# Kernel optimization log

Hardware: AMD Instinct MI355X
Metric: run time of the kernel (lower is better)

## Reference

```python
import jax, jax.numpy as jnp
import numpy as np

T, B, I, N, C = 2048, 512, 28, 256, 2
TAU = 2.0

def _lin_init(key, out_f, in_f):
    # torch nn.Linear default: U(-1/sqrt(in_f), 1/sqrt(in_f)) for weight and bias
    s = 1.0 / np.sqrt(in_f)
    kw, kb = jax.random.split(key)
    W = jax.random.uniform(kw, (out_f, in_f), jnp.float32, -s, s)
    b = jax.random.uniform(kb, (out_f,), jnp.float32, -s, s)
    return W, b

def setup_inputs() -> dict:
    key = jax.random.key(0)
    ks = jax.random.split(key, 8)
    data = jax.random.normal(ks[0], (T, B, I), jnp.float32)
    hier_signal = jax.random.normal(ks[1], (B, N), jnp.float32)
    h0 = 0.1 * jax.random.uniform(ks[2], (B, N), jnp.float32)  # matches 0.1*torch.rand init
    W_in, b_in = _lin_init(ks[3], N, I)   # input_layers[0]
    W_hh, b_hh = _lin_init(ks[4], N, N)   # w_hh[0]
    W_ff, b_ff = _lin_init(ks[5], N, N)   # w_ff_in
    W_fc, b_fc = _lin_init(ks[6], C, N)   # fc[0]
    return dict(data=data, hier_signal=hier_signal, h0=h0,
                W_in=W_in, b_in=b_in, W_hh=W_hh, b_hh=b_hh,
                W_ff=W_ff, b_ff=b_ff, W_fc=W_fc, b_fc=b_fc)

def reference(data, hier_signal, h0, W_in, b_in, W_hh, b_hh, W_ff, b_ff, W_fc, b_fc):
    # recurrent weight has its diagonal zeroed every forward call
    W_hh_z = W_hh * (1.0 - jnp.eye(W_hh.shape[0], dtype=W_hh.dtype))
    # input projection for all timesteps at once: [T,B,N]
    x = jnp.einsum('tbi,ni->tbn', data, W_in) + b_in
    # hierarchical feed-forward signal, constant over time: [B,N]
    ff = hier_signal @ W_ff.T + b_ff
    inv_tau = 1.0 / TAU
    keep = 1.0 - inv_tau

    def step(h, x_t):
        h = jax.nn.leaky_relu(keep * h + (h @ W_hh_z.T + b_hh + ff + x_t) * inv_tau)
        return h, None

    hT, _ = jax.lax.scan(step, h0, x)
    out = hT @ W_fc.T + b_fc  # readout head 0: [B, C]
    return out
```

## Files before the change

kernel.cpp:

```cpp
#include <hip/hip_runtime.h>
#include <stdint.h>
#include <stddef.h>

#define TSTEPS 2048
#define BATCH  512
#define IDIM   28
#define NDIM   256

typedef __attribute__((ext_vector_type(4))) float f32x4;
typedef __attribute__((ext_vector_type(8))) short short8;

#define MFMA __builtin_amdgcn_mfma_f32_16x16x32_bf16

__device__ __forceinline__ short8 pack2(f32x4 a, f32x4 b) {
  union { uint32_t u[4]; short8 s; } r;
  asm("v_cvt_pk_bf16_f32 %0, %1, %2" : "=v"(r.u[0]) : "v"(a[0]), "v"(a[1]));
  asm("v_cvt_pk_bf16_f32 %0, %1, %2" : "=v"(r.u[1]) : "v"(a[2]), "v"(a[3]));
  asm("v_cvt_pk_bf16_f32 %0, %1, %2" : "=v"(r.u[2]) : "v"(b[0]), "v"(b[1]));
  asm("v_cvt_pk_bf16_f32 %0, %1, %2" : "=v"(r.u[3]) : "v"(b[2]), "v"(b[3]));
  return r.s;
}

#define RNN_STEP(P, DLO, DHI, tcur)                                           \
  {                                                                           \
    short8 Bx = pack2(DLO, DHI);                                              \
    {                                                                         \
      int tt = (tcur) + 2; tt = (tt > TSTEPS - 1) ? (TSTEPS - 1) : tt;        \
      const float* rp = dptr + (size_t)tt * (BATCH * IDIM);                   \
      DLO = *(const f32x4*)rp;                                                \
      if (g < 3) DHI = *(const f32x4*)(rp + 16);                              \
    }                                                                         \
    const short8* rb = (const short8*)(&ldsf[(P)][0][0][0]);                  \
    short8 B0 = rb[0 * 64 + lane], B1 = rb[1 * 64 + lane];                    \
    short8 B2 = rb[2 * 64 + lane], B3 = rb[3 * 64 + lane];                    \
    short8 B4 = rb[4 * 64 + lane], B5 = rb[5 * 64 + lane];                    \
    short8 B6 = rb[6 * 64 + lane], B7 = rb[7 * 64 + lane];                    \
    f32x4 acc0, acc1;                                                         \
    _Pragma("unroll")                                                         \
    for (int r = 0; r < 4; ++r) {                                             \
      acc0[r] = __builtin_fmaf(0.5f, h0r[r], cst0[r]);                        \
      acc1[r] = __builtin_fmaf(0.5f, h1r[r], cst1[r]);                        \
    }                                                                         \
    acc0 = MFMA(A_hh0[0], B0, acc0, 0, 0, 0);                                 \
    acc1 = MFMA(A_hh1[0], B0, acc1, 0, 0, 0);                                 \
    acc0 = MFMA(A_hh0[1], B1, acc0, 0, 0, 0);                                 \
    acc1 = MFMA(A_hh1[1], B1, acc1, 0, 0, 0);                                 \
    acc0 = MFMA(A_hh0[2], B2, acc0, 0, 0, 0);                                 \
    acc1 = MFMA(A_hh1[2], B2, acc1, 0, 0, 0);                                 \
    acc0 = MFMA(A_hh0[3], B3, acc0, 0, 0, 0);                                 \
    acc1 = MFMA(A_hh1[3], B3, acc1, 0, 0, 0);                                 \
    acc0 = MFMA(A_hh0[4], B4, acc0, 0, 0, 0);                                 \
    acc1 = MFMA(A_hh1[4], B4, acc1, 0, 0, 0);                                 \
    acc0 = MFMA(A_hh0[5], B5, acc0, 0, 0, 0);                                 \
    acc1 = MFMA(A_hh1[5], B5, acc1, 0, 0, 0);                                 \
    acc0 = MFMA(A_hh0[6], B6, acc0, 0, 0, 0);                                 \
    acc1 = MFMA(A_hh1[6], B6, acc1, 0, 0, 0);                                 \
    acc0 = MFMA(A_hh0[7], B7, acc0, 0, 0, 0);                                 \
    acc1 = MFMA(A_hh1[7], B7, acc1, 0, 0, 0);                                 \
    acc0 = MFMA(A_in0, Bx, acc0, 0, 0, 0);                                    \
    acc1 = MFMA(A_in1, Bx, acc1, 0, 0, 0);                                    \
    _Pragma("unroll")                                                         \
    for (int r = 0; r < 4; ++r) {                                             \
      float p0 = acc0[r]; h0r[r] = __builtin_fmaxf(p0, 0.01f * p0);           \
      float p1 = acc1[r]; h1r[r] = __builtin_fmaxf(p1, 0.01f * p1);           \
    }                                                                         \
    ((short8*)(&ldsf[(P) ^ 1][0][0][0]))[wave * 64 + lane] = pack2(h0r, h1r); \
    __syncthreads();                                                          \
  }

__global__ __launch_bounds__(512)
void rnn_fused(const float* __restrict__ data,
               const float* __restrict__ hier,
               const float* __restrict__ h0,
               const float* __restrict__ W_in,
               const float* __restrict__ b_in,
               const float* __restrict__ W_hh,
               const float* __restrict__ b_hh,
               const float* __restrict__ W_ff,
               const float* __restrict__ b_ff,
               const float* __restrict__ W_fc,
               const float* __restrict__ b_fc,
               float* __restrict__ out)
{
  __shared__ short ldsf[2][8][64][8];
  __shared__ float ldsh[16][264];

  const int tid  = threadIdx.x;
  const int wave = tid >> 6;
  const int lane = tid & 63;
  const int g    = lane >> 4;
  const int c    = lane & 15;
  const int b0   = blockIdx.x * 16;

  const int m0 = 32 * wave + c;
  const int m1 = m0 + 16;

  f32x4 cst0 = {0.f, 0.f, 0.f, 0.f}, cst1 = {0.f, 0.f, 0.f, 0.f};
  {
    const float* hp = hier + (size_t)(b0 + c) * NDIM + 4 * g;
    const float* w0 = W_ff + (size_t)m0 * NDIM + 4 * g;
    const float* w1 = W_ff + (size_t)m1 * NDIM + 4 * g;
#pragma unroll
    for (int kt = 0; kt < 8; ++kt) {
      short8 bh  = pack2(*(const f32x4*)(hp + kt * 32), *(const f32x4*)(hp + kt * 32 + 16));
      short8 af0 = pack2(*(const f32x4*)(w0 + kt * 32), *(const f32x4*)(w0 + kt * 32 + 16));
      short8 af1 = pack2(*(const f32x4*)(w1 + kt * 32), *(const f32x4*)(w1 + kt * 32 + 16));
      cst0 = MFMA(af0, bh, cst0, 0, 0, 0);
      cst1 = MFMA(af1, bh, cst1, 0, 0, 0);
    }
  }
#pragma unroll
  for (int r = 0; r < 4; ++r) {
    int n0 = 32 * wave + 4 * g + r;
    int n1 = n0 + 16;
    cst0[r] = 0.5f * (cst0[r] + b_hh[n0] + b_in[n0] + b_ff[n0]);
    cst1[r] = 0.5f * (cst1[r] + b_hh[n1] + b_in[n1] + b_ff[n1]);
  }

  short8 A_hh0[8], A_hh1[8], A_in0, A_in1;
  {
    const float* w0 = W_hh + (size_t)m0 * NDIM + 4 * g;
    const float* w1 = W_hh + (size_t)m1 * NDIM + 4 * g;
#pragma unroll
    for (int kt = 0; kt < 8; ++kt) {
      f32x4 lo0 = *(const f32x4*)(w0 + kt * 32);
      f32x4 hi0 = *(const f32x4*)(w0 + kt * 32 + 16);
      f32x4 lo1 = *(const f32x4*)(w1 + kt * 32);
      f32x4 hi1 = *(const f32x4*)(w1 + kt * 32 + 16);
#pragma unroll
      for (int j = 0; j < 4; ++j) {
        int kl = kt * 32 + 4 * g + j, kh = kl + 16;
        lo0[j] = (kl == m0) ? 0.f : 0.5f * lo0[j];
        hi0[j] = (kh == m0) ? 0.f : 0.5f * hi0[j];
        lo1[j] = (kl == m1) ? 0.f : 0.5f * lo1[j];
        hi1[j] = (kh == m1) ? 0.f : 0.5f * hi1[j];
      }
      A_hh0[kt] = pack2(lo0, hi0);
      A_hh1[kt] = pack2(lo1, hi1);
    }
    const float* p0 = W_in + (size_t)m0 * IDIM;
    const float* p1 = W_in + (size_t)m1 * IDIM;
    f32x4 lo0 = *(const f32x4*)(p0 + 4 * g);
    f32x4 lo1 = *(const f32x4*)(p1 + 4 * g);
    f32x4 hi0 = {0.f, 0.f, 0.f, 0.f}, hi1 = {0.f, 0.f, 0.f, 0.f};
    if (g < 3) {
      hi0 = *(const f32x4*)(p0 + 16 + 4 * g);
      hi1 = *(const f32x4*)(p1 + 16 + 4 * g);
    }
#pragma unroll
    for (int j = 0; j < 4; ++j) {
      lo0[j] *= 0.5f; hi0[j] *= 0.5f; lo1[j] *= 0.5f; hi1[j] *= 0.5f;
    }
    A_in0 = pack2(lo0, hi0);
    A_in1 = pack2(lo1, hi1);
  }

  f32x4 h0r, h1r;
  {
    const float* hp = h0 + (size_t)(b0 + c) * NDIM + 32 * wave + 4 * g;
    h0r = *(const f32x4*)hp;
    h1r = *(const f32x4*)(hp + 16);
    ((short8*)(&ldsf[0][0][0][0]))[wave * 64 + lane] = pack2(h0r, h1r);
  }

  const float* dptr = data + (size_t)(b0 + c) * IDIM + 4 * g;
  f32x4 dlo0, dlo1;
  f32x4 dhi0 = {0.f, 0.f, 0.f, 0.f}, dhi1 = {0.f, 0.f, 0.f, 0.f};
  dlo0 = *(const f32x4*)dptr;
  dlo1 = *(const f32x4*)(dptr + (size_t)BATCH * IDIM);
  if (g < 3) {
    dhi0 = *(const f32x4*)(dptr + 16);
    dhi1 = *(const f32x4*)(dptr + (size_t)BATCH * IDIM + 16);
  }

  __syncthreads();

  for (int t = 0; t < TSTEPS; t += 2) {
    RNN_STEP(0, dlo0, dhi0, t)
    RNN_STEP(1, dlo1, dhi1, t + 1)
  }

  *(f32x4*)(&ldsh[c][32 * wave + 4 * g])      = h0r;
  *(f32x4*)(&ldsh[c][32 * wave + 16 + 4 * g]) = h1r;
  __syncthreads();
  if (tid < 32) {
    int b = tid >> 1, cls = tid & 1;
    float s = b_fc[cls];
    const float* wf = W_fc + (size_t)cls * NDIM;
#pragma unroll 8
    for (int n = 0; n < NDIM; ++n) s += ldsh[b][n] * wf[n];
    out[(size_t)(b0 + b) * 2 + cls] = s;
  }
}

extern "C" void kernel_launch(void* const* d_in, const int* in_sizes, int n_in,
                              void* d_out, int out_size, void* d_ws, size_t ws_size,
                              hipStream_t stream) {
  const float* data = (const float*)d_in[0];
  const float* hier = (const float*)d_in[1];
  const float* h0   = (const float*)d_in[2];
  const float* W_in = (const float*)d_in[3];
  const float* b_in = (const float*)d_in[4];
  const float* W_hh = (const float*)d_in[5];
  const float* b_hh = (const float*)d_in[6];
  const float* W_ff = (const float*)d_in[7];
  const float* b_ff = (const float*)d_in[8];
  const float* W_fc = (const float*)d_in[9];
  const float* b_fc = (const float*)d_in[10];
  rnn_fused<<<dim3(BATCH / 16), dim3(512), 0, stream>>>(
      data, hier, h0, W_in, b_in, W_hh, b_hh, W_ff, b_ff, W_fc, b_fc,
      (float*)d_out);
}
```

Before: 1.060 ms.

## Split MFMA accumulation chains, deepen input prefetch, use lightweight LDS barrier

Each step's matmul now runs as two independent accumulator chains per output tile, one per half of K, which are summed before the activation. This halves the dependent MFMA chain length on the serial recurrence critical path. The input prefetch distance grows from two to four timesteps with the loop unrolled by four. __syncthreads is replaced by a barrier that waits only on LDS counters, so outstanding global prefetches are not drained. The costs are extra registers and a small reassociation change in the floating-point sum.

```diff
diff --git a/kernel.cpp b/kernel.cpp
--- a/kernel.cpp
+++ b/kernel.cpp
@@ -21,51 +21,60 @@
   return r.s;
 }
 
+#define LDS_BARRIER()                                       \
+  do {                                                      \
+    __asm__ volatile("s_waitcnt lgkmcnt(0)" ::: "memory");  \
+    __builtin_amdgcn_s_barrier();                           \
+    __asm__ volatile("" ::: "memory");                      \
+  } while (0)
+
 #define RNN_STEP(P, DLO, DHI, tcur)                                           \
   {                                                                           \
     short8 Bx = pack2(DLO, DHI);                                              \
     {                                                                         \
-      int tt = (tcur) + 2; tt = (tt > TSTEPS - 1) ? (TSTEPS - 1) : tt;        \
+      int tt = (tcur) + 4; tt = (tt > TSTEPS - 1) ? (TSTEPS - 1) : tt;        \
       const float* rp = dptr + (size_t)tt * (BATCH * IDIM);                   \
       DLO = *(const f32x4*)rp;                                                \
       if (g < 3) DHI = *(const f32x4*)(rp + 16);                              \
     }                                                                         \
     const short8* rb = (const short8*)(&ldsf[(P)][0][0][0]);                  \
-    short8 B0 = rb[0 * 64 + lane], B1 = rb[1 * 64 + lane];                    \
-    short8 B2 = rb[2 * 64 + lane], B3 = rb[3 * 64 + lane];                    \
-    short8 B4 = rb[4 * 64 + lane], B5 = rb[5 * 64 + lane];                    \
-    short8 B6 = rb[6 * 64 + lane], B7 = rb[7 * 64 + lane];                    \
-    f32x4 acc0, acc1;                                                         \
+    short8 B0 = rb[0 * 64 + lane], B4 = rb[4 * 64 + lane];                    \
+    short8 B1 = rb[1 * 64 + lane], B5 = rb[5 * 64 + lane];                    \
+    short8 B2 = rb[2 * 64 + lane], B6 = rb[6 * 64 + lane];                    \
+    short8 B3 = rb[3 * 64 + lane], B7 = rb[7 * 64 + lane];                    \
+    f32x4 acc0a, acc1a;                                                       \
+    f32x4 acc0b = {0.f, 0.f, 0.f, 0.f}, acc1b = {0.f, 0.f, 0.f, 0.f};        \
     _Pragma("unroll")                                                         \
     for (int r = 0; r < 4; ++r) {                                             \
-      acc0[r] = __builtin_fmaf(0.5f, h0r[r], cst0[r]);                        \
-      acc1[r] = __builtin_fmaf(0.5f, h1r[r], cst1[r]);                        \
+      acc0a[r] = __builtin_fmaf(0.5f, h0r[r], cst0[r]);                       \
+      acc1a[r] = __builtin_fmaf(0.5f, h1r[r], cst1[r]);                       \
     }                                                                         \
-    acc0 = MFMA(A_hh0[0], B0, acc0, 0, 0, 0);                                 \
-    acc1 = MFMA(A_hh1[0], B0, acc1, 0, 0, 0);                                 \
-    acc0 = MFMA(A_hh0[1], B1, acc0, 0, 0, 0);                                 \
-    acc1 = MFMA(A_hh1[1], B1, acc1, 0, 0, 0);                                 \
-    acc0 = MFMA(A_hh0[2], B2, acc0, 0, 0, 0);                                 \
-    acc1 = MFMA(A_hh1[2], B2, acc1, 0, 0, 0);                                 \
-    acc0 = MFMA(A_hh0[3], B3, acc0, 0, 0, 0);                                 \
-    acc1 = MFMA(A_hh1[3], B3, acc1, 0, 0, 0);                                 \
-    acc0 = MFMA(A_hh0[4], B4, acc0, 0, 0, 0);                                 \
-    acc1 = MFMA(A_hh1[4], B4, acc1, 0, 0, 0);                                 \
-    acc0 = MFMA(A_hh0[5], B5, acc0, 0, 0, 0);                                 \
-    acc1 = MFMA(A_hh1[5], B5, acc1, 0, 0, 0);                                 \
-    acc0 = MFMA(A_hh0[6], B6, acc0, 0, 0, 0);                                 \
-    acc1 = MFMA(A_hh1[6], B6, acc1, 0, 0, 0);                                 \
-    acc0 = MFMA(A_hh0[7], B7, acc0, 0, 0, 0);                                 \
-    acc1 = MFMA(A_hh1[7], B7, acc1, 0, 0, 0);                                 \
-    acc0 = MFMA(A_in0, Bx, acc0, 0, 0, 0);                                    \
-    acc1 = MFMA(A_in1, Bx, acc1, 0, 0, 0);                                    \
+            \
+    acc0a = MFMA(A_hh0[0], B0, acc0a, 0, 0, 0);                               \
+    acc1a = MFMA(A_hh1[0], B0, acc1a, 0, 0, 0);                               \
+    acc0b = MFMA(A_hh0[4], B4, acc0b, 0, 0, 0);                               \
+    acc1b = MFMA(A_hh1[4], B4, acc1b, 0, 0, 0);                               \
+    acc0a = MFMA(A_hh0[1], B1, acc0a, 0, 0, 0);                               \
+    acc1a = MFMA(A_hh1[1], B1, acc1a, 0, 0, 0);                               \
+    acc0b = MFMA(A_hh0[5], B5, acc0b, 0, 0, 0);                               \
+    acc1b = MFMA(A_hh1[5], B5, acc1b, 0, 0, 0);                               \
+    acc0a = MFMA(A_hh0[2], B2, acc0a, 0, 0, 0);                               \
+    acc1a = MFMA(A_hh1[2], B2, acc1a, 0, 0, 0);                               \
+    acc0b = MFMA(A_hh0[6], B6, acc0b, 0, 0, 0);                               \
+    acc1b = MFMA(A_hh1[6], B6, acc1b, 0, 0, 0);                               \
+    acc0a = MFMA(A_hh0[3], B3, acc0a, 0, 0, 0);                               \
+    acc1a = MFMA(A_hh1[3], B3, acc1a, 0, 0, 0);                               \
+    acc0b = MFMA(A_hh0[7], B7, acc0b, 0, 0, 0);                               \
+    acc1b = MFMA(A_hh1[7], B7, acc1b, 0, 0, 0);                               \
+    acc0b = MFMA(A_in0, Bx, acc0b, 0, 0, 0);                                  \
+    acc1b = MFMA(A_in1, Bx, acc1b, 0, 0, 0);                                  \
     _Pragma("unroll")                                                         \
     for (int r = 0; r < 4; ++r) {                                             \
-      float p0 = acc0[r]; h0r[r] = __builtin_fmaxf(p0, 0.01f * p0);           \
-      float p1 = acc1[r]; h1r[r] = __builtin_fmaxf(p1, 0.01f * p1);           \
+      float p0 = acc0a[r] + acc0b[r]; h0r[r] = __builtin_fmaxf(p0, 0.01f * p0); \
+      float p1 = acc1a[r] + acc1b[r]; h1r[r] = __builtin_fmaxf(p1, 0.01f * p1); \
     }                                                                         \
     ((short8*)(&ldsf[(P) ^ 1][0][0][0]))[wave * 64 + lane] = pack2(h0r, h1r); \
-    __syncthreads();                                                          \
+    LDS_BARRIER();                                                            \
   }
 
 __global__ __launch_bounds__(512)
@@ -164,20 +173,27 @@
   }
 
   const float* dptr = data + (size_t)(b0 + c) * IDIM + 4 * g;
-  f32x4 dlo0, dlo1;
+  f32x4 dlo0, dlo1, dlo2, dlo3;
   f32x4 dhi0 = {0.f, 0.f, 0.f, 0.f}, dhi1 = {0.f, 0.f, 0.f, 0.f};
+  f32x4 dhi2 = {0.f, 0.f, 0.f, 0.f}, dhi3 = {0.f, 0.f, 0.f, 0.f};
   dlo0 = *(const f32x4*)dptr;
-  dlo1 = *(const f32x4*)(dptr + (size_t)BATCH * IDIM);
+  dlo1 = *(const f32x4*)(dptr + (size_t)1 * BATCH * IDIM);
+  dlo2 = *(const f32x4*)(dptr + (size_t)2 * BATCH * IDIM);
+  dlo3 = *(const f32x4*)(dptr + (size_t)3 * BATCH * IDIM);
   if (g < 3) {
     dhi0 = *(const f32x4*)(dptr + 16);
-    dhi1 = *(const f32x4*)(dptr + (size_t)BATCH * IDIM + 16);
+    dhi1 = *(const f32x4*)(dptr + (size_t)1 * BATCH * IDIM + 16);
+    dhi2 = *(const f32x4*)(dptr + (size_t)2 * BATCH * IDIM + 16);
+    dhi3 = *(const f32x4*)(dptr + (size_t)3 * BATCH * IDIM + 16);
   }
 
   __syncthreads();
 
-  for (int t = 0; t < TSTEPS; t += 2) {
+  for (int t = 0; t < TSTEPS; t += 4) {
     RNN_STEP(0, dlo0, dhi0, t)
     RNN_STEP(1, dlo1, dhi1, t + 1)
+    RNN_STEP(0, dlo2, dhi2, t + 2)
+    RNN_STEP(1, dlo3, dhi3, t + 3)
   }
 
   *(f32x4*)(&ldsh[c][32 * wave + 4 * g])      = h0r;
```

After: 1.021 ms. -3.7%, faster.

## Reorder recurrent MFMA chain to start from own h slice, deepen input prefetch

Applied to the files above, without the earlier changes.

Each wave now keeps its own packed h slice in registers and starts the MFMA chain with it, followed by the input projection. The remaining K-tiles are read from LDS in wave-rotated order, so the first MFMAs can issue before any LDS reads land and different waves hit different LDS rows. The input prefetch moves from two to four timesteps ahead using a pointer walk, with the hi-part offset trick (-4) replacing the conditional load. __syncthreads is replaced by an explicit lgkmcnt wait plus s_barrier, s_setprio raises priority around the MFMA block, and launch bounds add an occupancy hint. These aim to shorten the serial per-step latency of the recurrence, at the cost of more prefetch registers.

```diff
diff --git a/kernel.cpp b/kernel.cpp
--- a/kernel.cpp
+++ b/kernel.cpp
@@ -21,54 +21,61 @@
   return r.s;
 }
 
-#define RNN_STEP(P, DLO, DHI, tcur)                                           \
+#define LDS_BARRIER()                                       \
+  do {                                                      \
+    __asm__ volatile("s_waitcnt lgkmcnt(0)" ::: "memory");  \
+    __builtin_amdgcn_s_barrier();                           \
+    __asm__ volatile("" ::: "memory");                      \
+  } while (0)
+
+#define RNN_STEP(P, DLO, DHI, PF)                                             \
   {                                                                           \
+    const short8* rb = (const short8*)(&ldsf[(P)][0][0][0]);                  \
+    short8 Bf1 = rb[rd1], Bf2 = rb[rd2], Bf3 = rb[rd3], Bf4 = rb[rd4];        \
+    short8 Bf5 = rb[rd5], Bf6 = rb[rd6], Bf7 = rb[rd7];                       \
     short8 Bx = pack2(DLO, DHI);                                              \
-    {                                                                         \
-      int tt = (tcur) + 2; tt = (tt > TSTEPS - 1) ? (TSTEPS - 1) : tt;        \
-      const float* rp = dptr + (size_t)tt * (BATCH * IDIM);                   \
-      DLO = *(const f32x4*)rp;                                                \
-      if (g < 3) DHI = *(const f32x4*)(rp + 16);                              \
+    if (PF) {                                                                 \
+      DLO = *(const f32x4*)dpf;                                               \
+      DHI = *(const f32x4*)(dpf + hiOff);                                     \
+      dpf += BATCH * IDIM;                                                    \
     }                                                                         \
-    const short8* rb = (const short8*)(&ldsf[(P)][0][0][0]);                  \
-    short8 B0 = rb[0 * 64 + lane], B1 = rb[1 * 64 + lane];                    \
-    short8 B2 = rb[2 * 64 + lane], B3 = rb[3 * 64 + lane];                    \
-    short8 B4 = rb[4 * 64 + lane], B5 = rb[5 * 64 + lane];                    \
-    short8 B6 = rb[6 * 64 + lane], B7 = rb[7 * 64 + lane];                    \
     f32x4 acc0, acc1;                                                         \
     _Pragma("unroll")                                                         \
     for (int r = 0; r < 4; ++r) {                                             \
-      acc0[r] = __builtin_fmaf(0.5f, h0r[r], cst0[r]);                        \
-      acc1[r] = __builtin_fmaf(0.5f, h1r[r], cst1[r]);                        \
+      acc0[r] = __builtin_fmaf(0.5f, hc0[r], cst0[r]);                        \
+      acc1[r] = __builtin_fmaf(0.5f, hc1[r], cst1[r]);                        \
     }                                                                         \
-    acc0 = MFMA(A_hh0[0], B0, acc0, 0, 0, 0);                                 \
-    acc1 = MFMA(A_hh1[0], B0, acc1, 0, 0, 0);                                 \
-    acc0 = MFMA(A_hh0[1], B1, acc0, 0, 0, 0);                                 \
-    acc1 = MFMA(A_hh1[1], B1, acc1, 0, 0, 0);                                 \
-    acc0 = MFMA(A_hh0[2], B2, acc0, 0, 0, 0);                                 \
-    acc1 = MFMA(A_hh1[2], B2, acc1, 0, 0, 0);                                 \
-    acc0 = MFMA(A_hh0[3], B3, acc0, 0, 0, 0);                                 \
-    acc1 = MFMA(A_hh1[3], B3, acc1, 0, 0, 0);                                 \
-    acc0 = MFMA(A_hh0[4], B4, acc0, 0, 0, 0);                                 \
-    acc1 = MFMA(A_hh1[4], B4, acc1, 0, 0, 0);                                 \
-    acc0 = MFMA(A_hh0[5], B5, acc0, 0, 0, 0);                                 \
-    acc1 = MFMA(A_hh1[5], B5, acc1, 0, 0, 0);                                 \
-    acc0 = MFMA(A_hh0[6], B6, acc0, 0, 0, 0);                                 \
-    acc1 = MFMA(A_hh1[6], B6, acc1, 0, 0, 0);                                 \
-    acc0 = MFMA(A_hh0[7], B7, acc0, 0, 0, 0);                                 \
-    acc1 = MFMA(A_hh1[7], B7, acc1, 0, 0, 0);                                 \
-    acc0 = MFMA(A_in0, Bx, acc0, 0, 0, 0);                                    \
-    acc1 = MFMA(A_in1, Bx, acc1, 0, 0, 0);                                    \
+    __builtin_amdgcn_s_setprio(1);                                            \
+    acc0 = MFMA(A_hh[0][0], Bown, acc0, 0, 0, 0);                             \
+    acc1 = MFMA(A_hh[1][0], Bown, acc1, 0, 0, 0);                             \
+    acc0 = MFMA(A_in[0], Bx, acc0, 0, 0, 0);                                  \
+    acc1 = MFMA(A_in[1], Bx, acc1, 0, 0, 0);                                  \
+    acc0 = MFMA(A_hh[0][1], Bf1, acc0, 0, 0, 0);                              \
+    acc1 = MFMA(A_hh[1][1], Bf1, acc1, 0, 0, 0);                              \
+    acc0 = MFMA(A_hh[0][2], Bf2, acc0, 0, 0, 0);                              \
+    acc1 = MFMA(A_hh[1][2], Bf2, acc1, 0, 0, 0);                              \
+    acc0 = MFMA(A_hh[0][3], Bf3, acc0, 0, 0, 0);                              \
+    acc1 = MFMA(A_hh[1][3], Bf3, acc1, 0, 0, 0);                              \
+    acc0 = MFMA(A_hh[0][4], Bf4, acc0, 0, 0, 0);                              \
+    acc1 = MFMA(A_hh[1][4], Bf4, acc1, 0, 0, 0);                              \
+    acc0 = MFMA(A_hh[0][5], Bf5, acc0, 0, 0, 0);                              \
+    acc1 = MFMA(A_hh[1][5], Bf5, acc1, 0, 0, 0);                              \
+    acc0 = MFMA(A_hh[0][6], Bf6, acc0, 0, 0, 0);                              \
+    acc1 = MFMA(A_hh[1][6], Bf6, acc1, 0, 0, 0);                              \
+    acc0 = MFMA(A_hh[0][7], Bf7, acc0, 0, 0, 0);                              \
+    acc1 = MFMA(A_hh[1][7], Bf7, acc1, 0, 0, 0);                              \
+    __builtin_amdgcn_s_setprio(0);                                            \
     _Pragma("unroll")                                                         \
     for (int r = 0; r < 4; ++r) {                                             \
-      float p0 = acc0[r]; h0r[r] = __builtin_fmaxf(p0, 0.01f * p0);           \
-      float p1 = acc1[r]; h1r[r] = __builtin_fmaxf(p1, 0.01f * p1);           \
+      float p0 = acc0[r]; hc0[r] = __builtin_fmaxf(p0, 0.01f * p0);           \
+      float p1 = acc1[r]; hc1[r] = __builtin_fmaxf(p1, 0.01f * p1);           \
     }                                                                         \
-    ((short8*)(&ldsf[(P) ^ 1][0][0][0]))[wave * 64 + lane] = pack2(h0r, h1r); \
-    __syncthreads();                                                          \
-  }
-
-__global__ __launch_bounds__(512)
+    Bown = pack2(hc0, hc1);                                                   \
+    ((short8*)(&ldsf[(P) ^ 1][0][0][0]))[wr] = Bown;                          \
+    LDS_BARRIER();                                                            \
+  }
+
+__global__ __launch_bounds__(512, 2)
 void rnn_fused(const float* __restrict__ data,
                const float* __restrict__ hier,
                const float* __restrict__ h0,
@@ -82,7 +89,7 @@
                const float* __restrict__ b_fc,
                float* __restrict__ out)
 {
-  __shared__ short ldsf[2][8][64][8];
+  __shared__ __attribute__((aligned(16))) short ldsf[2][8][64][8];
   __shared__ float ldsh[16][264];
 
   const int tid  = threadIdx.x;
@@ -95,7 +102,16 @@
   const int m0 = 32 * wave + c;
   const int m1 = m0 + 16;
 
-  f32x4 cst0 = {0.f, 0.f, 0.f, 0.f}, cst1 = {0.f, 0.f, 0.f, 0.f};
+  const int wr  = wave * 64 + lane;
+  const int rd1 = ((wave + 1) & 7) * 64 + lane;
+  const int rd2 = ((wave + 2) & 7) * 64 + lane;
+  const int rd3 = ((wave + 3) & 7) * 64 + lane;
+  const int rd4 = ((wave + 4) & 7) * 64 + lane;
+  const int rd5 = ((wave + 5) & 7) * 64 + lane;
+  const int rd6 = ((wave + 6) & 7) * 64 + lane;
+  const int rd7 = ((wave + 7) & 7) * 64 + lane;
+
+  f32x4 cst0 = {0.f,0.f,0.f,0.f}, cst1 = {0.f,0.f,0.f,0.f};
   {
     const float* hp = hier + (size_t)(b0 + c) * NDIM + 4 * g;
     const float* w0 = W_ff + (size_t)m0 * NDIM + 4 * g;
@@ -111,77 +127,72 @@
   }
 #pragma unroll
   for (int r = 0; r < 4; ++r) {
-    int n0 = 32 * wave + 4 * g + r;
-    int n1 = n0 + 16;
-    cst0[r] = 0.5f * (cst0[r] + b_hh[n0] + b_in[n0] + b_ff[n0]);
-    cst1[r] = 0.5f * (cst1[r] + b_hh[n1] + b_in[n1] + b_ff[n1]);
-  }
-
-  short8 A_hh0[8], A_hh1[8], A_in0, A_in1;
-  {
-    const float* w0 = W_hh + (size_t)m0 * NDIM + 4 * g;
-    const float* w1 = W_hh + (size_t)m1 * NDIM + 4 * g;
-#pragma unroll
-    for (int kt = 0; kt < 8; ++kt) {
-      f32x4 lo0 = *(const f32x4*)(w0 + kt * 32);
-      f32x4 hi0 = *(const f32x4*)(w0 + kt * 32 + 16);
-      f32x4 lo1 = *(const f32x4*)(w1 + kt * 32);
-      f32x4 hi1 = *(const f32x4*)(w1 + kt * 32 + 16);
-#pragma unroll
-      for (int j = 0; j < 4; ++j) {
-        int kl = kt * 32 + 4 * g + j, kh = kl + 16;
-        lo0[j] = (kl == m0) ? 0.f : 0.5f * lo0[j];
-        hi0[j] = (kh == m0) ? 0.f : 0.5f * hi0[j];
-        lo1[j] = (kl == m1) ? 0.f : 0.5f * lo1[j];
-        hi1[j] = (kh == m1) ? 0.f : 0.5f * hi1[j];
+    const int n0 = 32 * wave + 4 * g + r;
+    cst0[r] = 0.5f * (cst0[r] + b_hh[n0]      + b_in[n0]      + b_ff[n0]);
+    cst1[r] = 0.5f * (cst1[r] + b_hh[n0 + 16] + b_in[n0 + 16] + b_ff[n0 + 16]);
+  }
+
+  short8 A_hh[2][8];
+  short8 A_in[2];
+#pragma unroll
+  for (int i = 0; i < 2; ++i) {
+    const int row = 32 * wave + 16 * i + c;
+    const float* wrow = W_hh + (size_t)row * NDIM;
+#pragma unroll
+    for (int j = 0; j < 8; ++j) {
+      const int ktg = (wave + j) & 7;
+      f32x4 lo = *(const f32x4*)(wrow + 32 * ktg + 4 * g);
+      f32x4 hi = *(const f32x4*)(wrow + 32 * ktg + 16 + 4 * g);
+#pragma unroll
+      for (int q = 0; q < 4; ++q) {
+        const int kl = 32 * ktg + 4 * g + q, kh = kl + 16;
+        lo[q] = (kl == row) ? 0.f : 0.5f * lo[q];
+        hi[q] = (kh == row) ? 0.f : 0.5f * hi[q];
       }
-      A_hh0[kt] = pack2(lo0, hi0);
-      A_hh1[kt] = pack2(lo1, hi1);
+      A_hh[i][j] = pack2(lo, hi);
     }
-    const float* p0 = W_in + (size_t)m0 * IDIM;
-    const float* p1 = W_in + (size_t)m1 * IDIM;
-    f32x4 lo0 = *(const f32x4*)(p0 + 4 * g);
-    f32x4 lo1 = *(const f32x4*)(p1 + 4 * g);
-    f32x4 hi0 = {0.f, 0.f, 0.f, 0.f}, hi1 = {0.f, 0.f, 0.f, 0.f};
-    if (g < 3) {
-      hi0 = *(const f32x4*)(p0 + 16 + 4 * g);
-      hi1 = *(const f32x4*)(p1 + 16 + 4 * g);
-    }
-#pragma unroll
-    for (int j = 0; j < 4; ++j) {
-      lo0[j] *= 0.5f; hi0[j] *= 0.5f; lo1[j] *= 0.5f; hi1[j] *= 0.5f;
-    }
-    A_in0 = pack2(lo0, hi0);
-    A_in1 = pack2(lo1, hi1);
-  }
-
-  f32x4 h0r, h1r;
+    const float* p = W_in + (size_t)row * IDIM;
+    f32x4 lo = *(const f32x4*)(p + 4 * g);
+    f32x4 hi = {0.f, 0.f, 0.f, 0.f};
+    if (g < 3) hi = *(const f32x4*)(p + 16 + 4 * g);
+#pragma unroll
+    for (int q = 0; q < 4; ++q) { lo[q] *= 0.5f; hi[q] *= 0.5f; }
+    A_in[i] = pack2(lo, hi);
+  }
+
+  f32x4 hc0, hc1;
+  short8 Bown;
   {
     const float* hp = h0 + (size_t)(b0 + c) * NDIM + 32 * wave + 4 * g;
-    h0r = *(const f32x4*)hp;
-    h1r = *(const f32x4*)(hp + 16);
-    ((short8*)(&ldsf[0][0][0][0]))[wave * 64 + lane] = pack2(h0r, h1r);
-  }
-
-  const float* dptr = data + (size_t)(b0 + c) * IDIM + 4 * g;
-  f32x4 dlo0, dlo1;
-  f32x4 dhi0 = {0.f, 0.f, 0.f, 0.f}, dhi1 = {0.f, 0.f, 0.f, 0.f};
-  dlo0 = *(const f32x4*)dptr;
-  dlo1 = *(const f32x4*)(dptr + (size_t)BATCH * IDIM);
-  if (g < 3) {
-    dhi0 = *(const f32x4*)(dptr + 16);
-    dhi1 = *(const f32x4*)(dptr + (size_t)BATCH * IDIM + 16);
-  }
+    hc0 = *(const f32x4*)(hp + 0);
+    hc1 = *(const f32x4*)(hp + 16);
+    Bown = pack2(hc0, hc1);
+    ((short8*)(&ldsf[0][0][0][0]))[wr] = Bown;
+  }
+
+  const int hiOff = (g < 3) ? 16 : -4;
+  const float* dpf = data + (size_t)(b0 + c) * IDIM + 4 * g;
+  f32x4 dlo0, dlo1, dlo2, dlo3, dhi0, dhi1, dhi2, dhi3;
+  dlo0 = *(const f32x4*)dpf; dhi0 = *(const f32x4*)(dpf + hiOff); dpf += BATCH * IDIM;
+  dlo1 = *(const f32x4*)dpf; dhi1 = *(const f32x4*)(dpf + hiOff); dpf += BATCH * IDIM;
+  dlo2 = *(const f32x4*)dpf; dhi2 = *(const f32x4*)(dpf + hiOff); dpf += BATCH * IDIM;
+  dlo3 = *(const f32x4*)dpf; dhi3 = *(const f32x4*)(dpf + hiOff); dpf += BATCH * IDIM;
 
   __syncthreads();
 
-  for (int t = 0; t < TSTEPS; t += 2) {
-    RNN_STEP(0, dlo0, dhi0, t)
-    RNN_STEP(1, dlo1, dhi1, t + 1)
-  }
-
-  *(f32x4*)(&ldsh[c][32 * wave + 4 * g])      = h0r;
-  *(f32x4*)(&ldsh[c][32 * wave + 16 + 4 * g]) = h1r;
+  for (int t = 0; t < TSTEPS - 4; t += 4) {
+    RNN_STEP(0, dlo0, dhi0, 1)
+    RNN_STEP(1, dlo1, dhi1, 1)
+    RNN_STEP(0, dlo2, dhi2, 1)
+    RNN_STEP(1, dlo3, dhi3, 1)
+  }
+  RNN_STEP(0, dlo0, dhi0, 0)
+  RNN_STEP(1, dlo1, dhi1, 0)
+  RNN_STEP(0, dlo2, dhi2, 0)
+  RNN_STEP(1, dlo3, dhi3, 0)
+
+  *(f32x4*)(&ldsh[c][32 * wave + 4 * g])      = hc0;
+  *(f32x4*)(&ldsh[c][32 * wave + 16 + 4 * g]) = hc1;
   __syncthreads();
   if (tid < 32) {
     int b = tid >> 1, cls = tid & 1;
```

After: 1.049 ms. About the same (-1.0%).
